# Kernel tuning notes

Hardware: AMD Instinct MI355X
Metric: run time of the kernel (lower is better)

Reference implementation:

```python
import jax, jax.numpy as jnp
import numpy as np

B, N, D, H = 2, 2048, 1024, 16
DK = D // H


def setup_inputs() -> dict:
    key = jax.random.key(0)
    ks = jax.random.split(key, 12)
    s = D ** -0.5
    inp = {
        "query": jax.random.normal(ks[0], (B, N, D), jnp.float32),
        "key": jax.random.normal(ks[1], (B, N, D), jnp.float32),
        "value": jax.random.normal(ks[2], (B, N, D), jnp.float32),
        # causal mask: 1 = keep, 0 = masked (matches create_causal_mask)
        "mask": jnp.tril(jnp.ones((N, N), jnp.int32)),
        "Wq": jax.random.normal(ks[3], (D, D), jnp.float32) * s,
        "bq": jnp.zeros((D,), jnp.float32),
        "Wk": jax.random.normal(ks[4], (D, D), jnp.float32) * s,
        "bk": jnp.zeros((D,), jnp.float32),
        "Wv": jax.random.normal(ks[5], (D, D), jnp.float32) * s,
        "bv": jnp.zeros((D,), jnp.float32),
        "Wo": jax.random.normal(ks[6], (D, D), jnp.float32) * s,
        "bo": jnp.zeros((D,), jnp.float32),
    }
    return inp


def reference(query, key, value, mask, Wq, bq, Wk, bk, Wv, bv, Wo, bo):
    scale = DK ** -0.5
    # Linear projections (torch nn.Linear: x @ W.T + b), split into heads -> [B,H,N,DK]
    q = (query @ Wq.T + bq).reshape(B, N, H, DK).transpose(0, 2, 1, 3)
    k = (key @ Wk.T + bk).reshape(B, N, H, DK).transpose(0, 2, 1, 3)
    v = (value @ Wv.T + bv).reshape(B, N, H, DK).transpose(0, 2, 1, 3)
    scores = jnp.einsum("bhqd,bhkd->bhqk", q, k) * scale  # [B,H,N,N]
    scores = jnp.where(mask[None, None, :, :] == 0, jnp.float32(-1e9), scores)
    attn = jax.nn.softmax(scores, axis=-1)
    ctx = jnp.einsum("bhqk,bhkd->bhqd", attn, v)  # [B,H,N,DK]
    ctx = ctx.transpose(0, 2, 1, 3).reshape(B, N, D)
    return ctx @ Wo.T + bo
```

## Files before the change

kernel.cpp:

```cpp
#include <hip/hip_runtime.h>
#include <hip/hip_bf16.h>

typedef __attribute__((ext_vector_type(4))) float f32x4;
typedef __attribute__((ext_vector_type(8))) __bf16 bf16x8;
typedef __attribute__((ext_vector_type(8))) unsigned short u16x8;
typedef __attribute__((ext_vector_type(4))) unsigned short u16x4;
typedef __attribute__((ext_vector_type(2))) unsigned int u32x2;
typedef unsigned short u16;

#define DEV static __device__ __forceinline__

DEV u16 f2bf(float f){
  unsigned u = __builtin_bit_cast(unsigned, f);
  u += 0x7fff + ((u >> 16) & 1);
  return (u16)(u >> 16);
}

DEV f32x4 mfma16(bf16x8 a, bf16x8 b, f32x4 c){
  return __builtin_amdgcn_mfma_f32_16x16x32_bf16(a, b, c, 0, 0, 0);
}

DEV void gload16(const void* g, void* l){
  __builtin_amdgcn_global_load_lds((const __attribute__((address_space(1))) void*)g,
                                   (__attribute__((address_space(3))) void*)l,
                                   16, 0, 0);
}

DEV float fexp2(float x){
#if __has_builtin(__builtin_amdgcn_exp2f)
  return __builtin_amdgcn_exp2f(x);
#else
  float r; asm("v_exp_f32 %0, %1" : "=v"(r) : "v"(x)); return r;
#endif
}

#define SCL 0.18033688011f
#define THR 11.0f
#define PLD 72

__global__ __launch_bounds__(256) void cvt_k(
    const float* __restrict__ s0, const float* __restrict__ s1,
    const float* __restrict__ s2, const float* __restrict__ s3,
    const float* __restrict__ s4, const float* __restrict__ s5,
    const float* __restrict__ s6,
    u16* __restrict__ d0, u16* __restrict__ d1, u16* __restrict__ d2,
    u16* __restrict__ d3, u16* __restrict__ d4, u16* __restrict__ d5,
    u16* __restrict__ d6){
  const int y = blockIdx.y;
  const float* __restrict__ s = y==0?s0:y==1?s1:y==2?s2:y==3?s3:y==4?s4:y==5?s5:s6;
  u16* __restrict__ d         = y==0?d0:y==1?d1:y==2?d2:y==3?d3:y==4?d4:y==5?d5:d6;
  const int n8 = (y < 3) ? (4096*1024/8) : (1024*1024/8);
  for (int i = blockIdx.x*256 + threadIdx.x; i < n8; i += gridDim.x*256){
    f32x4 a = *(const f32x4*)&s[(size_t)i*8];
    f32x4 b = *(const f32x4*)&s[(size_t)i*8 + 4];
    u16x8 h;
    #pragma unroll
    for (int j = 0; j < 4; ++j){ h[j] = f2bf(a[j]); h[j+4] = f2bf(b[j]); }
    *(u16x8*)&d[(size_t)i*8] = h;
  }
}

DEV bf16x8 rdS(const u16* T, int r, int kc, int lhi){
  int gr = (kc*4 + lhi) ^ (r & 7);
  return *(const bf16x8*)&T[r*64 + gr*8];
}

__global__ __launch_bounds__(256) void gemm_qkv3(
    const u16* __restrict__ Xq, const u16* __restrict__ Xk, const u16* __restrict__ Xv,
    const u16* __restrict__ Wq, const u16* __restrict__ Wk, const u16* __restrict__ Wv,
    const float* __restrict__ Bq, const float* __restrict__ Bk, const float* __restrict__ Bv,
    u16* __restrict__ Oq, u16* __restrict__ Ok, u16* __restrict__ Ov){
  __shared__ u16 As[128*64];
  __shared__ u16 Bs[128*64];

  const int f = blockIdx.x;
  const int xc = f & 7, g = f >> 3;
  const int p  = xc*12 + (g >> 3);
  const int bn8 = g & 7;
  const int z = p >> 5, bm32 = p & 31;
  const bool vt = (z == 2);
  const int bm = vt ? bn8 : bm32;
  const int bn = vt ? bm32 : bn8;

  const u16* __restrict__ A    = z==0 ? Xq : z==1 ? Xk : Wv;
  const u16* __restrict__ Bw   = z==0 ? Wq : z==1 ? Wk : Xv;
  const float* __restrict__ bias = z==0 ? Bq : z==1 ? Bk : Bv;
  u16* __restrict__ C = z==0 ? Oq : z==1 ? Ok : Ov;
  const float qs = (z==0) ? SCL : 1.0f;

  const int tid = threadIdx.x, lane = tid & 63, w = tid >> 6;
  const int wr = w >> 1, wc = w & 1;
  const int l16 = lane & 15, lhi = lane >> 4;

  const u16* Asrc[4];
  const u16* Bsrc[4];
  #pragma unroll
  for (int j = 0; j < 4; ++j){
    int s = tid + j*256;
    int row = s >> 3;
    int col = ((s & 7) ^ (row & 7)) * 8;
    Asrc[j] = A  + (size_t)(bm*128 + row)*1024 + col;
    Bsrc[j] = Bw + (size_t)(bn*128 + row)*1024 + col;
  }

  f32x4 acc[4][4] = {};

  for (int k0 = 0; k0 < 1024; k0 += 64){
    __syncthreads();
    #pragma unroll
    for (int j = 0; j < 4; ++j)
      gload16(Asrc[j] + k0, As + (tid + j*256)*8);
    #pragma unroll
    for (int j = 0; j < 4; ++j)
      gload16(Bsrc[j] + k0, Bs + (tid + j*256)*8);
    __syncthreads();

    #pragma unroll
    for (int kc = 0; kc < 2; ++kc){
      bf16x8 af[4], bfr[4];
      #pragma unroll
      for (int mi = 0; mi < 4; ++mi)
        af[mi] = rdS(As, wr*64 + mi*16 + l16, kc, lhi);
      #pragma unroll
      for (int nf = 0; nf < 4; ++nf)
        bfr[nf] = rdS(Bs, wc*64 + nf*16 + l16, kc, lhi);
      #pragma unroll
      for (int mi = 0; mi < 4; ++mi)
        #pragma unroll
        for (int nf = 0; nf < 4; ++nf)
          acc[mi][nf] = mfma16(af[mi], bfr[nf], acc[mi][nf]);
    }
  }

  #pragma unroll
  for (int mi = 0; mi < 4; ++mi){
    #pragma unroll
    for (int nf = 0; nf < 4; ++nf){
      int row0 = bm*128 + wr*64 + mi*16 + lhi*4;
      int col  = bn*128 + wc*64 + nf*16 + l16;
      float bc = bias[col];
      #pragma unroll
      for (int r = 0; r < 4; ++r){
        int row = row0 + r;
        float val = (acc[mi][nf][r] + (vt ? bias[row] : bc)) * qs;
        if (!vt){
          int b = row >> 11, n = row & 2047;
          int h = col >> 6,  dk = col & 63;
          C[(((size_t)(b*16 + h))*2048 + n)*64 + dk] = f2bf(val);
        } else {
          int h = row >> 6,  dk = row & 63;
          int b = col >> 11, n = col & 2047;
          C[(((size_t)(b*16 + h))*64 + dk)*2048 + n] = f2bf(val);
        }
      }
    }
  }
}

__global__ __launch_bounds__(256) void gemm_o64(const u16* __restrict__ A,
                                                const u16* __restrict__ Bw,
                                                const float* __restrict__ bias,
                                                float* __restrict__ C){
  __shared__ u16 As[64*32];
  __shared__ u16 Bs[128*32];
  const int f = blockIdx.x;
  const int bm = (f & 7)*8 + ((f >> 3) >> 3);
  const int bn = (f >> 3) & 7;
  const int tid  = threadIdx.x;
  const int lane = tid & 63, w = tid >> 6;
  const int wr = w >> 1, wc = w & 1;
  const int l16 = lane & 15, lhi = lane >> 4;

  const int srow = w*16 + (lane >> 2);
  const int scol = (lane & 3)*8;
  const u16* Asrc = A  + (size_t)(bm*64  + srow)*1024 + scol;
  const u16* Bsrc = Bw + (size_t)(bn*128 + srow)*1024 + scol;
  u16* Adst0 = As + w*512;
  u16* Bdst0 = Bs + w*512;

  f32x4 acc[2][4] = {};

  for (int k0 = 0; k0 < 1024; k0 += 32){
    __syncthreads();
    gload16(Asrc + k0,             Adst0);
    gload16(Bsrc + k0,             Bdst0);
    gload16(Bsrc + 64*1024 + k0,   Bdst0 + 2048);
    __syncthreads();

    bf16x8 af[2], bfr[4];
    #pragma unroll
    for (int mi = 0; mi < 2; ++mi)
      af[mi] = *(const bf16x8*)&As[(wr*32 + mi*16 + l16)*32 + lhi*8];
    #pragma unroll
    for (int nf = 0; nf < 4; ++nf)
      bfr[nf] = *(const bf16x8*)&Bs[(wc*64 + nf*16 + l16)*32 + lhi*8];
    #pragma unroll
    for (int mi = 0; mi < 2; ++mi)
      #pragma unroll
      for (int nf = 0; nf < 4; ++nf)
        acc[mi][nf] = mfma16(af[mi], bfr[nf], acc[mi][nf]);
  }

  #pragma unroll
  for (int mi = 0; mi < 2; ++mi){
    #pragma unroll
    for (int nf = 0; nf < 4; ++nf){
      int row0 = bm*64 + wr*32 + mi*16 + lhi*4;
      int col  = bn*128 + wc*64 + nf*16 + l16;
      float bv = bias[col];
      #pragma unroll
      for (int r = 0; r < 4; ++r)
        C[(size_t)(row0 + r)*1024 + col] = acc[mi][nf][r] + bv;
    }
  }
}

DEV void sm_tile(int t, int qt, int q_abs,
                 const u16* __restrict__ Ksb, u16* __restrict__ PsW,
                 bf16x8 bq0, bf16x8 bq1,
                 f32x4* ctx, float& m_r, float& l_r,
                 int l16, int lhi, int lane, int swz){
  f32x4 s4[4] = {};
  #pragma unroll
  for (int nf = 0; nf < 4; ++nf){
    bf16x8 ak0 = *(const bf16x8*)&Ksb[(nf*16 + l16)*64 + ((lhi*8) ^ swz)];
    bf16x8 ak1 = *(const bf16x8*)&Ksb[(nf*16 + l16)*64 + ((32 + lhi*8) ^ swz)];
    s4[nf] = mfma16(ak0, bq0, s4[nf]);
    s4[nf] = mfma16(ak1, bq1, s4[nf]);
  }

  if (t == qt){
    #pragma unroll
    for (int nf = 0; nf < 4; ++nf)
      #pragma unroll
      for (int r = 0; r < 4; ++r){
        int kc = t*64 + nf*16 + lhi*4 + r;
        if (kc > q_abs) s4[nf][r] = -1.0e30f;
      }
  }

  float mt = fmaxf(
      fmaxf(fmaxf(fmaxf(s4[0][0],s4[0][1]), fmaxf(s4[0][2],s4[0][3])),
            fmaxf(fmaxf(s4[1][0],s4[1][1]), fmaxf(s4[1][2],s4[1][3]))),
      fmaxf(fmaxf(fmaxf(s4[2][0],s4[2][1]), fmaxf(s4[2][2],s4[2][3])),
            fmaxf(fmaxf(s4[3][0],s4[3][1]), fmaxf(s4[3][2],s4[3][3]))));
  mt = fmaxf(mt, __shfl_xor(mt, 16));
  mt = fmaxf(mt, __shfl_xor(mt, 32));

  if (!__all(mt <= m_r + THR)){
    float mn = fmaxf(m_r, mt);
    float sf = fexp2(m_r - mn);
    m_r = mn;
    l_r *= sf;
    float sfb[4];
    #pragma unroll
    for (int r = 0; r < 4; ++r)
      sfb[r] = __shfl(sf, (lane >> 4)*4 + r);
    #pragma unroll
    for (int dkf = 0; dkf < 4; ++dkf)
      #pragma unroll
      for (int r = 0; r < 4; ++r)
        ctx[dkf][r] *= sfb[r];
  }

  float lt = 0.f;
  u16* prow = PsW + l16*PLD;
  #pragma unroll
  for (int nf = 0; nf < 4; ++nf){
    float p0 = fexp2(s4[nf][0] - m_r);
    float p1 = fexp2(s4[nf][1] - m_r);
    float p2 = fexp2(s4[nf][2] - m_r);
    float p3 = fexp2(s4[nf][3] - m_r);
    lt += (p0 + p1) + (p2 + p3);
    unsigned w0 = __builtin_amdgcn_perm(__builtin_bit_cast(unsigned, p1),
                                        __builtin_bit_cast(unsigned, p0), 0x07060302u);
    unsigned w1 = __builtin_amdgcn_perm(__builtin_bit_cast(unsigned, p3),
                                        __builtin_bit_cast(unsigned, p2), 0x07060302u);
    u32x2 wp = {w0, w1};
    *(u32x2*)&prow[nf*16 + lhi*4] = wp;
  }
  lt += __shfl_xor(lt, 16);
  lt += __shfl_xor(lt, 32);
  l_r += lt;
}

DEV void pv_tile(const u16* __restrict__ Vsb, const u16* __restrict__ PsW,
                 f32x4* ctx, int l16, int lhi, int swz){
  const u16* prow = PsW + l16*PLD;
  __builtin_amdgcn_s_setprio(1);
  #pragma unroll
  for (int ks = 0; ks < 2; ++ks){
    bf16x8 pa = *(const bf16x8*)&prow[ks*32 + lhi*8];
    #pragma unroll
    for (int dkf = 0; dkf < 4; ++dkf){
      bf16x8 vb = *(const bf16x8*)&Vsb[(dkf*16 + l16)*64 + ((ks*32 + lhi*8) ^ swz)];
      ctx[dkf] = mfma16(pa, vb, ctx[dkf]);
    }
  }
  __builtin_amdgcn_s_setprio(0);
}

__global__ __launch_bounds__(256) void attn_k(const u16* __restrict__ Q,
                                              const u16* __restrict__ K,
                                              const u16* __restrict__ Vt,
                                              u16* __restrict__ CTX){
  __shared__ u16 Ks[2][64*64];
  __shared__ u16 Vs[2][64*64];
  __shared__ u16 Ps[4][2][16*PLD];
  const int tid  = threadIdx.x;
  const int lane = tid & 63, w = tid >> 6;
  const int l16 = lane & 15, lhi = lane >> 4;
  const int f  = blockIdx.x;
  const int bh = f & 31;
  const int qt = 31 - (f >> 5);
  const size_t base = (size_t)bh * 2048 * 64;
  const u16* Qb = Q  + base;
  const u16* Kb = K  + base;
  const u16* Vb = Vt + base;
  const int b = bh >> 4, h = bh & 15;

  const int s0 = tid, s1 = tid + 256;
  const int r0 = s0 >> 3, c0 = ((s0 & 7) ^ (r0 & 7))*8;
  const int r1 = s1 >> 3, c1 = ((s1 & 7) ^ (r1 & 7))*8;
  const u16* Ksrc0 = Kb + r0*64 + c0;
  const u16* Ksrc1 = Kb + r1*64 + c1;
  const u16* Vsrc0 = Vb + (size_t)r0*2048 + c0;
  const u16* Vsrc1 = Vb + (size_t)r1*2048 + c1;
  const int swz = (l16 & 7)*8;

  const int q_abs = qt*64 + w*16 + l16;
  bf16x8 bq0 = *(const bf16x8*)&Qb[(size_t)q_abs*64 + lhi*8];
  bf16x8 bq1 = *(const bf16x8*)&Qb[(size_t)q_abs*64 + 32 + lhi*8];

  f32x4 ctx[4] = {};
  float m_r = -3.0e38f, l_r = 0.f;
  u16* Ps0 = &Ps[w][0][0];
  u16* Ps1 = &Ps[w][1][0];

  gload16(Ksrc0, &Ks[0][s0*8]);  gload16(Ksrc1, &Ks[0][s1*8]);
  gload16(Vsrc0, &Vs[0][s0*8]);  gload16(Vsrc1, &Vs[0][s1*8]);
  __syncthreads();

  const int nt = qt + 1;
  for (int t = 0; t < nt; ++t){
    const int pb = t & 1;
    u16* PsC = pb ? Ps1 : Ps0;
    u16* PsP = pb ? Ps0 : Ps1;
    if (t + 1 < nt){
      gload16(Ksrc0 + (t+1)*4096, &Ks[pb^1][s0*8]);
      gload16(Ksrc1 + (t+1)*4096, &Ks[pb^1][s1*8]);
    }
    sm_tile(t, qt, q_abs, Ks[pb], PsC, bq0, bq1, ctx, m_r, l_r, l16, lhi, lane, swz);
    if (t > 0)
      pv_tile(Vs[pb^1], PsP, ctx, l16, lhi, swz);
    __syncthreads();
    if (t + 1 < nt){
      gload16(Vsrc0 + (size_t)(t+1)*64, &Vs[pb^1][s0*8]);
      gload16(Vsrc1 + (size_t)(t+1)*64, &Vs[pb^1][s1*8]);
    }
  }
  pv_tile(Vs[(nt-1)&1], (nt-1)&1 ? Ps1 : Ps0, ctx, l16, lhi, swz);

  float lf[4];
  #pragma unroll
  for (int r = 0; r < 4; ++r)
    lf[r] = __shfl(l_r, (lane >> 4)*4 + r);
  #pragma unroll
  for (int dkf = 0; dkf < 4; ++dkf)
    #pragma unroll
    for (int r = 0; r < 4; ++r){
      int q = qt*64 + w*16 + lhi*4 + r;
      CTX[((size_t)(b*2048 + q))*1024 + h*64 + dkf*16 + l16] = f2bf(ctx[dkf][r] / lf[r]);
    }
}

extern "C" void kernel_launch(void* const* d_in, const int* in_sizes, int n_in,
                              void* d_out, int out_size, void* d_ws, size_t ws_size,
                              hipStream_t stream){
  const float* q  = (const float*)d_in[0];
  const float* k  = (const float*)d_in[1];
  const float* v  = (const float*)d_in[2];
  const float* Wq = (const float*)d_in[4];  const float* bq = (const float*)d_in[5];
  const float* Wk = (const float*)d_in[6];  const float* bk = (const float*)d_in[7];
  const float* Wv = (const float*)d_in[8];  const float* bv = (const float*)d_in[9];
  const float* Wo = (const float*)d_in[10]; const float* bo = (const float*)d_in[11];
  float* out = (float*)d_out;
  dim3 blk(256);

  u16* Wqb = (u16*)d_ws;
  u16* Wkb = Wqb + 1048576;
  u16* Wvb = Wkb + 1048576;
  u16* Wob = Wvb + 1048576;
  u16* Xqb = Wob + 1048576;
  u16* Xkb = Xqb + 4194304;
  u16* Xvb = Xkb + 4194304;
  u16* Qw  = Xvb + 4194304;
  u16* Kw  = Qw + 4194304;
  u16* Vw  = Kw + 4194304;
  u16* Cw  = Xqb;

  cvt_k<<<dim3(512, 7), blk, 0, stream>>>(q, k, v, Wq, Wk, Wv, Wo,
                                          Xqb, Xkb, Xvb, Wqb, Wkb, Wvb, Wob);
  gemm_qkv3<<<dim3(768), blk, 0, stream>>>(Xqb, Xkb, Xvb, Wqb, Wkb, Wvb,
                                           bq, bk, bv, Qw, Kw, Vw);
  attn_k<<<dim3(1024), blk, 0, stream>>>(Qw, Kw, Vw, Cw);
  gemm_o64<<<dim3(512), blk, 0, stream>>>(Cw, Wob, bo, out);
}
```

Measured before the change: 133.1 us.

## Double-buffer LDS in projection GEMMs and drop swizzled XCD block mapping

Both the QKV projection GEMM and the output GEMM now use two LDS buffers, so the next K-slice loads while MFMAs run on the current one, with one barrier per iteration instead of two. The QKV GEMM also goes from a 64-wide K step with an XOR-swizzled LDS layout to a 32-wide unswizzled step. Both kernels drop the XCD-aware block remapping in favour of a plain 2D/3D grid. The trade-offs are possible LDS bank conflicts from the unswizzled layout, double the number of K iterations, and possibly worse L2 locality across XCDs.

```diff
diff --git a/kernel.cpp b/kernel.cpp
--- a/kernel.cpp
+++ b/kernel.cpp
@@ -60,76 +60,64 @@
   }
 }
 
-DEV bf16x8 rdS(const u16* T, int r, int kc, int lhi){
-  int gr = (kc*4 + lhi) ^ (r & 7);
-  return *(const bf16x8*)&T[r*64 + gr*8];
-}
-
-__global__ __launch_bounds__(256) void gemm_qkv3(
-    const u16* __restrict__ Xq, const u16* __restrict__ Xk, const u16* __restrict__ Xv,
-    const u16* __restrict__ Wq, const u16* __restrict__ Wk, const u16* __restrict__ Wv,
-    const float* __restrict__ Bq, const float* __restrict__ Bk, const float* __restrict__ Bv,
-    u16* __restrict__ Oq, u16* __restrict__ Ok, u16* __restrict__ Ov){
-  __shared__ u16 As[128*64];
-  __shared__ u16 Bs[128*64];
-
-  const int f = blockIdx.x;
-  const int xc = f & 7, g = f >> 3;
-  const int p  = xc*12 + (g >> 3);
-  const int bn8 = g & 7;
-  const int z = p >> 5, bm32 = p & 31;
+__global__ __launch_bounds__(256) void gemm_bt(
+    const u16* __restrict__ A0, const u16* __restrict__ A1, const u16* __restrict__ A2,
+    const u16* __restrict__ B0, const u16* __restrict__ B1, const u16* __restrict__ B2,
+    const float* __restrict__ e0, const float* __restrict__ e1, const float* __restrict__ e2,
+    u16* __restrict__ C0, u16* __restrict__ C1, u16* __restrict__ C2){
+  __shared__ u16 As[2][128*32];
+  __shared__ u16 Bs[2][128*32];
+  const int z = blockIdx.z;
+  const u16* __restrict__ A    = z==0 ? A0 : z==1 ? A1 : A2;
+  const u16* __restrict__ Bw   = z==0 ? B0 : z==1 ? B1 : B2;
+  const float* __restrict__ bias = z==0 ? e0 : z==1 ? e1 : e2;
+  u16* __restrict__ C          = z==0 ? C0 : z==1 ? C1 : C2;
   const bool vt = (z == 2);
-  const int bm = vt ? bn8 : bm32;
-  const int bn = vt ? bm32 : bn8;
-
-  const u16* __restrict__ A    = z==0 ? Xq : z==1 ? Xk : Wv;
-  const u16* __restrict__ Bw   = z==0 ? Wq : z==1 ? Wk : Xv;
-  const float* __restrict__ bias = z==0 ? Bq : z==1 ? Bk : Bv;
-  u16* __restrict__ C = z==0 ? Oq : z==1 ? Ok : Ov;
-  const float qs = (z==0) ? SCL : 1.0f;
-
-  const int tid = threadIdx.x, lane = tid & 63, w = tid >> 6;
+  const float qs = (z == 0) ? SCL : 1.0f;
+
+  const int tid  = threadIdx.x;
+  const int lane = tid & 63, w = tid >> 6;
   const int wr = w >> 1, wc = w & 1;
   const int l16 = lane & 15, lhi = lane >> 4;
-
-  const u16* Asrc[4];
-  const u16* Bsrc[4];
-  #pragma unroll
-  for (int j = 0; j < 4; ++j){
-    int s = tid + j*256;
-    int row = s >> 3;
-    int col = ((s & 7) ^ (row & 7)) * 8;
-    Asrc[j] = A  + (size_t)(bm*128 + row)*1024 + col;
-    Bsrc[j] = Bw + (size_t)(bn*128 + row)*1024 + col;
-  }
+  const int bm = vt ? blockIdx.x : blockIdx.y;
+  const int bn = vt ? blockIdx.y : blockIdx.x;
+
+  const int srow = w*16 + (lane >> 2);
+  const int scol = (lane & 3)*8;
+  const u16* Asrc = A  + (size_t)(bm*128 + srow)*1024 + scol;
+  const u16* Bsrc = Bw + (size_t)(bn*128 + srow)*1024 + scol;
+  const int d0 = w*512;
 
   f32x4 acc[4][4] = {};
 
-  for (int k0 = 0; k0 < 1024; k0 += 64){
+  gload16(Asrc,             &As[0][d0]);
+  gload16(Asrc + 64*1024,   &As[0][d0 + 2048]);
+  gload16(Bsrc,             &Bs[0][d0]);
+  gload16(Bsrc + 64*1024,   &Bs[0][d0 + 2048]);
+  __syncthreads();
+
+  for (int t = 0; t < 32; ++t){
+    const int cur = t & 1, nxt = cur ^ 1;
+    if (t < 31){
+      const int k1 = (t + 1)*32;
+      gload16(Asrc + k1,           &As[nxt][d0]);
+      gload16(Asrc + 64*1024 + k1, &As[nxt][d0 + 2048]);
+      gload16(Bsrc + k1,           &Bs[nxt][d0]);
+      gload16(Bsrc + 64*1024 + k1, &Bs[nxt][d0 + 2048]);
+    }
+    bf16x8 af[4], bfr[4];
+    #pragma unroll
+    for (int mi = 0; mi < 4; ++mi)
+      af[mi] = *(const bf16x8*)&As[cur][(wr*64 + mi*16 + l16)*32 + lhi*8];
+    #pragma unroll
+    for (int nf = 0; nf < 4; ++nf)
+      bfr[nf] = *(const bf16x8*)&Bs[cur][(wc*64 + nf*16 + l16)*32 + lhi*8];
+    #pragma unroll
+    for (int mi = 0; mi < 4; ++mi)
+      #pragma unroll
+      for (int nf = 0; nf < 4; ++nf)
+        acc[mi][nf] = mfma16(af[mi], bfr[nf], acc[mi][nf]);
     __syncthreads();
-    #pragma unroll
-    for (int j = 0; j < 4; ++j)
-      gload16(Asrc[j] + k0, As + (tid + j*256)*8);
-    #pragma unroll
-    for (int j = 0; j < 4; ++j)
-      gload16(Bsrc[j] + k0, Bs + (tid + j*256)*8);
-    __syncthreads();
-
-    #pragma unroll
-    for (int kc = 0; kc < 2; ++kc){
-      bf16x8 af[4], bfr[4];
-      #pragma unroll
-      for (int mi = 0; mi < 4; ++mi)
-        af[mi] = rdS(As, wr*64 + mi*16 + l16, kc, lhi);
-      #pragma unroll
-      for (int nf = 0; nf < 4; ++nf)
-        bfr[nf] = rdS(Bs, wc*64 + nf*16 + l16, kc, lhi);
-      #pragma unroll
-      for (int mi = 0; mi < 4; ++mi)
-        #pragma unroll
-        for (int nf = 0; nf < 4; ++nf)
-          acc[mi][nf] = mfma16(af[mi], bfr[nf], acc[mi][nf]);
-    }
   }
 
   #pragma unroll
@@ -161,44 +149,48 @@
                                                 const u16* __restrict__ Bw,
                                                 const float* __restrict__ bias,
                                                 float* __restrict__ C){
-  __shared__ u16 As[64*32];
-  __shared__ u16 Bs[128*32];
-  const int f = blockIdx.x;
-  const int bm = (f & 7)*8 + ((f >> 3) >> 3);
-  const int bn = (f >> 3) & 7;
+  __shared__ u16 As[2][64*32];
+  __shared__ u16 Bs[2][128*32];
   const int tid  = threadIdx.x;
   const int lane = tid & 63, w = tid >> 6;
   const int wr = w >> 1, wc = w & 1;
   const int l16 = lane & 15, lhi = lane >> 4;
+  const int bm = blockIdx.y, bn = blockIdx.x;
 
   const int srow = w*16 + (lane >> 2);
   const int scol = (lane & 3)*8;
   const u16* Asrc = A  + (size_t)(bm*64  + srow)*1024 + scol;
   const u16* Bsrc = Bw + (size_t)(bn*128 + srow)*1024 + scol;
-  u16* Adst0 = As + w*512;
-  u16* Bdst0 = Bs + w*512;
+  const int d0 = w*512;
 
   f32x4 acc[2][4] = {};
 
-  for (int k0 = 0; k0 < 1024; k0 += 32){
-    __syncthreads();
-    gload16(Asrc + k0,             Adst0);
-    gload16(Bsrc + k0,             Bdst0);
-    gload16(Bsrc + 64*1024 + k0,   Bdst0 + 2048);
-    __syncthreads();
-
+  gload16(Asrc,           &As[0][d0]);
+  gload16(Bsrc,           &Bs[0][d0]);
+  gload16(Bsrc + 64*1024, &Bs[0][d0 + 2048]);
+  __syncthreads();
+
+  for (int t = 0; t < 32; ++t){
+    const int cur = t & 1, nxt = cur ^ 1;
+    if (t < 31){
+      const int k1 = (t + 1)*32;
+      gload16(Asrc + k1,           &As[nxt][d0]);
+      gload16(Bsrc + k1,           &Bs[nxt][d0]);
+      gload16(Bsrc + 64*1024 + k1, &Bs[nxt][d0 + 2048]);
+    }
     bf16x8 af[2], bfr[4];
     #pragma unroll
     for (int mi = 0; mi < 2; ++mi)
-      af[mi] = *(const bf16x8*)&As[(wr*32 + mi*16 + l16)*32 + lhi*8];
+      af[mi] = *(const bf16x8*)&As[cur][(wr*32 + mi*16 + l16)*32 + lhi*8];
     #pragma unroll
     for (int nf = 0; nf < 4; ++nf)
-      bfr[nf] = *(const bf16x8*)&Bs[(wc*64 + nf*16 + l16)*32 + lhi*8];
+      bfr[nf] = *(const bf16x8*)&Bs[cur][(wc*64 + nf*16 + l16)*32 + lhi*8];
     #pragma unroll
     for (int mi = 0; mi < 2; ++mi)
       #pragma unroll
       for (int nf = 0; nf < 4; ++nf)
         acc[mi][nf] = mfma16(af[mi], bfr[nf], acc[mi][nf]);
+    __syncthreads();
   }
 
   #pragma unroll
@@ -401,8 +393,8 @@
 
   cvt_k<<<dim3(512, 7), blk, 0, stream>>>(q, k, v, Wq, Wk, Wv, Wo,
                                           Xqb, Xkb, Xvb, Wqb, Wkb, Wvb, Wob);
-  gemm_qkv3<<<dim3(768), blk, 0, stream>>>(Xqb, Xkb, Xvb, Wqb, Wkb, Wvb,
-                                           bq, bk, bv, Qw, Kw, Vw);
+  gemm_bt<<<dim3(8, 32, 3), blk, 0, stream>>>(
+      Xqb, Xkb, Wvb, Wqb, Wkb, Xvb, bq, bk, bv, Qw, Kw, Vw);
   attn_k<<<dim3(1024), blk, 0, stream>>>(Qw, Kw, Vw, Cw);
-  gemm_o64<<<dim3(512), blk, 0, stream>>>(Cw, Wob, bo, out);
-}
+  gemm_o64<<<dim3(8, 64), blk, 0, stream>>>(Cw, Wob, bo, out);
+}
```

New measurement: 131.1 us. Within noise of the previous version (-1.5%).
